# Optimization experiments

Hardware: AMD Instinct MI355X
Metric: run time of the kernel (lower is better)

Reference implementation:

```python
import jax, jax.numpy as jnp
from jax import lax
import numpy as np

N, D, H, ENT = 32768, 16, 128, 50000


def setup_inputs() -> dict:
    key = jax.random.key(0)
    ks = jax.random.split(key, 10)
    s = 0.05  # weight scale to keep tanh/sigmoid in active range
    return {
        "ent_table": jax.random.normal(ks[0], (ENT, H), jnp.float32) * s,
        "op_table": jax.random.normal(ks[1], (5, H), jnp.float32) * s,
        "non_table": jax.random.normal(ks[2], (1, H), jnp.float32) * s,
        "Wm": jax.random.normal(ks[3], (H, 3 * H), jnp.float32) * s,
        "bm": jnp.zeros((H,), jnp.float32),
        "Wg": jax.random.normal(ks[4], (H, 3 * H), jnp.float32) * s,
        "bg": jnp.zeros((H,), jnp.float32),
        "ops_idx": jax.random.randint(ks[5], (N, D), 0, 4, jnp.int32),
        "ents_idx": jax.random.randint(ks[6], (N, D + 1), 0, ENT, jnp.int32),
        "left_idx": jax.random.randint(ks[7], (N,), 0, ENT, jnp.int32),
    }


def reference(ent_table, op_table, non_table, Wm, bm, Wg, bg, ops_idx, ents_idx, left_idx):
    # Merge module (dropout in eval mode = identity):
    #   tanh(Linear([node, t1, t2])) * sigmoid(Linear_g([node, t1, t2]))
    def merge(node, t1, t2):
        x = jnp.concatenate([node, t1, t2], axis=-1)  # [N, 3H]
        return jnp.tanh(x @ Wm.T + bm) * jax.nn.sigmoid(x @ Wg.T + bg)

    op_e = op_table[ops_idx]        # [N, D, H]
    ent_e = ent_table[ents_idx]     # [N, D+1, H]

    # Right-leaning prefix tree: acc starts at deepest entity, merge upward.
    acc0 = ent_e[:, -1]             # [N, H]
    # scan over depth, from innermost (i = D-1) to outermost (i = 0)
    xs = (jnp.flip(op_e, axis=1).transpose(1, 0, 2),          # [D, N, H]
          jnp.flip(ent_e[:, :-1], axis=1).transpose(1, 0, 2))  # [D, N, H]

    def step(acc, inp):
        o, e = inp
        return merge(o, e, acc), None

    acc, _ = lax.scan(step, acc0, xs)

    eq_e = jnp.broadcast_to(op_table[4], acc.shape)  # '=' embedding, [N, H]
    left_e = ent_table[left_idx]                     # [N, H]
    score = merge(eq_e, left_e, acc)                 # [N, H]

    # all_score = cat(per-formula scores, non_embed)  -> [N+1, H]
    return jnp.concatenate([score, non_table], axis=0)
```

## Files before the change

kernel.cpp:

```cpp
#include <hip/hip_runtime.h>
#include <hip/hip_bf16.h>
#include <hip/hip_fp16.h>

#define NROWS 32768
#define HH 128
#define ENTN 50000

typedef _Float16 f16x8 __attribute__((ext_vector_type(8)));
typedef __fp16 fp16x2 __attribute__((ext_vector_type(2)));
typedef float f32x4 __attribute__((ext_vector_type(4)));
typedef float f32x16 __attribute__((ext_vector_type(16)));

#define OFF_PEB 0
#define OFF_WF  25600000
#define OFF_PEF (OFF_WF + 65536)
#define OFF_POPK (OFF_PEF + 65536)

#define KM 2.8853901f
#define KG (-1.4426950f)
#define RSTR 272
#define HALF (32 * RSTR)
#define TILEB (2 * HALF)

#if defined(__has_builtin)
#if __has_builtin(__builtin_amdgcn_exp2f)
#define FEXP2(x) __builtin_amdgcn_exp2f(x)
#endif
#endif
#ifndef FEXP2
__device__ __forceinline__ float __fexp2_asm(float x) {
    float r; asm("v_exp_f32 %0, %1" : "=v"(r) : "v"(x)); return r;
}
#define FEXP2(x) __fexp2_asm(x)
#endif

__device__ __forceinline__ unsigned pk2(float a, float b) {
    fp16x2 h = __builtin_amdgcn_cvt_pkrtz(a, b);
    unsigned u; __builtin_memcpy(&u, &h, 4); return u;
}
__device__ __forceinline__ unsigned pk2rtn(float a, float b) {
    _Float16 lo = (_Float16)a, hi = (_Float16)b;
    unsigned short ul, uh;
    __builtin_memcpy(&ul, &lo, 2); __builtin_memcpy(&uh, &hi, 2);
    return (unsigned)ul | ((unsigned)uh << 16);
}

__global__ void prep_kernel(const float* __restrict__ op_table,
                            const float* __restrict__ non_table,
                            const float* __restrict__ Wm, const float* __restrict__ bm,
                            const float* __restrict__ Wg, const float* __restrict__ bg,
                            char* __restrict__ ws, float* __restrict__ out) {
    int idx = blockIdx.x * blockDim.x + threadIdx.x;
    if (idx < 32768) {
        int e = idx;
        int jj = e & 7, l = (e >> 3) & 63, kt = (e >> 9) & 7, jb = e >> 12;
        int j = jb * 32 + (l & 31);
        int c = j >> 1, p = j & 1;
        int k = kt * 16 + (l >> 5) * 8 + jj;
        const float* Wrow = p ? (Wg + (size_t)c * 384) : (Wm + (size_t)c * 384);
        ((_Float16*)(ws + OFF_WF))[e] = (_Float16)(Wrow[256 + k] * (p ? KG : KM));
    } else if (idx < 65536) {
        int e = idx - 32768;
        int jj = e & 7, l = (e >> 3) & 63, kt = (e >> 9) & 3, jbf = e >> 11;
        int fr = l & 15;
        int j = (jbf >> 1) * 32 + 8 * (fr >> 2) + 4 * (jbf & 1) + (fr & 3);
        int c = j >> 1, p = j & 1;
        int k = kt * 32 + (l >> 4) * 8 + jj;
        const float* Wrow = p ? (Wg + (size_t)c * 384) : (Wm + (size_t)c * 384);
        ((_Float16*)(ws + OFF_PEF))[e] = (_Float16)Wrow[128 + k];
    } else if (idx < 66176) {
        int t2 = idx - 65536;
        int pr = t2 & 1, q = (t2 >> 1) & 3, h = (t2 >> 3) & 1, jb = (t2 >> 4) & 7, o = t2 >> 7;
        int j0 = jb * 32 + 8 * q + 4 * h + 2 * pr;
        int c = j0 >> 1;
        float sm = bm[c], sg = bg[c];
        const float* Wrm = Wm + (size_t)c * 384;
        const float* Wrg = Wg + (size_t)c * 384;
        for (int i = 0; i < 128; ++i) {
            float ov = op_table[o * HH + i];
            sm += ov * Wrm[i];
            sg += ov * Wrg[i];
        }
        ((unsigned*)(ws + OFF_POPK))[t2] = pk2rtn(sm * KM, sg * KG);
    } else if (idx < 66304) {
        int j = idx - 66176;
        out[(size_t)NROWS * HH + j] = non_table[j];
    }
}

__global__ __launch_bounds__(256, 4)
void pe_kernel(const float* __restrict__ ent_table, char* __restrict__ ws) {
    const f16x8* PEF = (const f16x8*)(ws + OFF_PEF);
    char* PEB = ws + OFF_PEB;
    int tid = threadIdx.x, w = tid >> 6, l = tid & 63, lr = l & 15, lg = (l >> 4) & 3;
    int e0 = blockIdx.x * 32;

    f16x8 WB[4][4];
    #pragma unroll
    for (int u = 0; u < 4; ++u)
        #pragma unroll
        for (int kt = 0; kt < 4; ++kt)
            WB[u][kt] = PEF[((4 * w + u) * 4 + kt) * 64 + l];

    f32x4 C[2][4];
    #pragma unroll
    for (int rt = 0; rt < 2; ++rt)
        #pragma unroll
        for (int u = 0; u < 4; ++u) C[rt][u] = (f32x4){0.f, 0.f, 0.f, 0.f};

    #pragma unroll
    for (int kt = 0; kt < 4; ++kt) {
        #pragma unroll
        for (int rt = 0; rt < 2; ++rt) {
            int e = e0 + rt * 16 + lr;
            if (e >= ENTN) e = ENTN - 1;
            const float4* s = (const float4*)(ent_table + (size_t)e * HH + kt * 32 + lg * 8);
            float4 v0 = s[0], v1 = s[1];
            unsigned u4[4] = {pk2(v0.x, v0.y), pk2(v0.z, v0.w),
                              pk2(v1.x, v1.y), pk2(v1.z, v1.w)};
            f16x8 A; __builtin_memcpy(&A, u4, 16);
            #pragma unroll
            for (int u = 0; u < 4; ++u)
                C[rt][u] = __builtin_amdgcn_mfma_f32_16x16x32_f16(WB[u][kt], A, C[rt][u], 0, 0, 0);
        }
    }
    #pragma unroll
    for (int rt = 0; rt < 2; ++rt) {
        int e = e0 + rt * 16 + lr;
        if (e < ENTN) {
            #pragma unroll
            for (int u = 0; u < 4; ++u) {
                int jb2 = 2 * w + (u >> 1);
                uint2 st;
                st.x = pk2(C[rt][u][0] * KM, C[rt][u][1] * KG);
                st.y = pk2(C[rt][u][2] * KM, C[rt][u][3] * KG);
                *(uint2*)(PEB + (size_t)e * 512 + jb2 * 64 + (u & 1) * 32 + lg * 8) = st;
            }
        }
    }
}

__global__ __launch_bounds__(512, 4)
void chain_kernel(const float* __restrict__ ent_table,
                  const int* __restrict__ ops_idx,
                  const int* __restrict__ ents_idx,
                  const int* __restrict__ left_idx,
                  const char* __restrict__ ws, float* __restrict__ out) {
    __shared__ char Abuf[4 * HALF];
    __shared__ unsigned eo[17 * 64];
    __shared__ unsigned popk[640];

    const char* PEBc = ws + OFF_PEB;
    const f16x8* WFp = (const f16x8*)(ws + OFF_WF);
    const unsigned* POPKg = (const unsigned*)(ws + OFF_POPK);

    int tid = threadIdx.x;
    int jb = tid >> 6, l = tid & 63, r = l & 31, h = l >> 5;
    int row0 = blockIdx.x * 64;

    for (int i = tid; i < 17 * 64; i += 512) {
        int t = i >> 6, rr = i & 63;
        unsigned e, o;
        if (t < 16) {
            e = ents_idx[(row0 + rr) * 17 + 15 - t];
            o = ops_idx[(row0 + rr) * 16 + 15 - t];
        } else {
            e = left_idx[row0 + rr];
            o = 4;
        }
        eo[i] = (e << 9) | o;
    }
    for (int i = tid; i < 640; i += 512) popk[i] = POPKg[i];

    f16x8 WH[8];
    #pragma unroll
    for (int kt = 0; kt < 8; ++kt)
        WH[kt] = WFp[(jb * 8 + kt) * 64 + l];

    {
        int rr = tid >> 3, sub = tid & 7;
        int e = ents_idx[(row0 + rr) * 17 + 16];
        const float4* src = (const float4*)(ent_table + (size_t)e * HH + sub * 16);
        float4 a = src[0], b = src[1], c2 = src[2], d2 = src[3];
        uint4 lo, hi;
        lo.x = pk2(a.x, a.y);  lo.y = pk2(a.z, a.w);
        lo.z = pk2(b.x, b.y);  lo.w = pk2(b.z, b.w);
        hi.x = pk2(c2.x, c2.y); hi.y = pk2(c2.z, c2.w);
        hi.z = pk2(d2.x, d2.y); hi.w = pk2(d2.z, d2.w);
        char* dst = Abuf + (rr >> 5) * TILEB + (rr & 31) * RSTR + sub * 32;
        *(uint4*)dst = lo;
        *(uint4*)(dst + 16) = hi;
    }
    __syncthreads();

    int rb = r * RSTR + h * 16;
    int wb = r * RSTR + jb * 32 + h * 4;
    const char* pebBase = PEBc + jb * 64 + h * 32;
    const char* popkB = (const char*)popk + jb * 64 + h * 32;
    const unsigned* eoB = eo + r;

    unsigned vaA = eoB[0], vaB = eoB[32];
    uint4 pa0A = *(const uint4*)(pebBase + (vaA & 0xFFFFFE00u));
    uint4 pa1A = *(const uint4*)(pebBase + (vaA & 0xFFFFFE00u) + 16);
    uint4 pa0B = *(const uint4*)(pebBase + (vaB & 0xFFFFFE00u));
    uint4 pa1B = *(const uint4*)(pebBase + (vaB & 0xFFFFFE00u) + 16);

#define TILE_BODY(VA, PA0, PA1, TOFF, ROWOFF, RD, WR, FINAL)                    \
    {                                                                           \
        const char* pq = popkB + ((VA) & 7u) * 512;                             \
        uint4 po0 = *(const uint4*)(pq);                                        \
        uint4 po1 = *(const uint4*)(pq + 16);                                   \
        unsigned pe_u[8] = {(PA0).x, (PA0).y, (PA0).z, (PA0).w,                 \
                            (PA1).x, (PA1).y, (PA1).z, (PA1).w};                \
        unsigned po_u[8] = {po0.x, po0.y, po0.z, po0.w,                         \
                            po1.x, po1.y, po1.z, po1.w};                        \
        f32x16 C;                                                               \
        _Pragma("unroll")                                                       \
        for (int q = 0; q < 4; ++q)                                             \
            _Pragma("unroll")                                                   \
            for (int pr = 0; pr < 2; ++pr) {                                    \
                int u = q * 2 + pr;                                             \
                __half2 sa = *(const __half2*)&pe_u[u];                         \
                __half2 sb = *(const __half2*)&po_u[u];                         \
                __half2 s = __hadd2(sa, sb);                                    \
                C[4 * q + 2 * pr] = __low2float(s);                             \
                C[4 * q + 2 * pr + 1] = __high2float(s);                        \
            }                                                                   \
        _Pragma("unroll")                                                       \
        for (int kt = 0; kt < 8; ++kt) {                                        \
            f16x8 A = *(const f16x8*)(Abuf + (TOFF) + rb + (RD) + kt * 32);     \
            C = __builtin_amdgcn_mfma_f32_32x32x16_f16(WH[kt], A, C, 0, 0, 0);  \
        }                                                                       \
        _Pragma("unroll")                                                       \
        for (int q = 0; q < 4; ++q) {                                           \
            float ov[2];                                                        \
            _Pragma("unroll")                                                   \
            for (int pr = 0; pr < 2; ++pr) {                                    \
                float m = C[4 * q + 2 * pr];                                    \
                float g = C[4 * q + 2 * pr + 1];                                \
                float em = FEXP2(m), eg = FEXP2(g);                             \
                ov[pr] = (em - 1.f) * __builtin_amdgcn_rcpf((em + 1.f) * (1.f + eg)); \
            }                                                                   \
            if (FINAL) {                                                        \
                *(float2*)(out + (size_t)(row0 + (ROWOFF) + r) * HH             \
                           + jb * 16 + 4 * q + 2 * h) = make_float2(ov[0], ov[1]); \
            } else {                                                            \
                *(unsigned*)(Abuf + (TOFF) + wb + (WR) + q * 8) = pk2(ov[0], ov[1]); \
            }                                                                   \
        }                                                                       \
    }

#define DO_STEP(T, RD, WR, FINAL)                                               \
    {                                                                           \
        uint4 npa0A, npa1A, npa0B, npa1B; unsigned nvaA = 0, nvaB = 0;          \
        if (!(FINAL)) {                                                         \
            nvaA = eoB[((T) + 1) * 64];                                         \
            nvaB = eoB[((T) + 1) * 64 + 32];                                    \
            npa0A = *(const uint4*)(pebBase + (nvaA & 0xFFFFFE00u));            \
            npa1A = *(const uint4*)(pebBase + (nvaA & 0xFFFFFE00u) + 16);       \
            npa0B = *(const uint4*)(pebBase + (nvaB & 0xFFFFFE00u));            \
            npa1B = *(const uint4*)(pebBase + (nvaB & 0xFFFFFE00u) + 16);       \
        }                                                                       \
        TILE_BODY(vaA, pa0A, pa1A, 0, 0, RD, WR, FINAL)                         \
        TILE_BODY(vaB, pa0B, pa1B, TILEB, 32, RD, WR, FINAL)                    \
        __syncthreads();                                                        \
        if (!(FINAL)) {                                                         \
            pa0A = npa0A; pa1A = npa1A; vaA = nvaA;                             \
            pa0B = npa0B; pa1B = npa1B; vaB = nvaB;                             \
        }                                                                       \
    }

    for (int tb = 0; tb < 8; ++tb) {
        int t0 = 2 * tb;
        DO_STEP(t0, 0, HALF, 0)
        DO_STEP(t0 + 1, HALF, 0, 0)
    }
    DO_STEP(16, 0, HALF, 1)
#undef DO_STEP
#undef TILE_BODY
}

extern "C" void kernel_launch(void* const* d_in, const int* in_sizes, int n_in,
                              void* d_out, int out_size, void* d_ws, size_t ws_size,
                              hipStream_t stream) {
    const float* ent_table = (const float*)d_in[0];
    const float* op_table  = (const float*)d_in[1];
    const float* non_table = (const float*)d_in[2];
    const float* Wm        = (const float*)d_in[3];
    const float* bm        = (const float*)d_in[4];
    const float* Wg        = (const float*)d_in[5];
    const float* bg        = (const float*)d_in[6];
    const int* ops_idx     = (const int*)d_in[7];
    const int* ents_idx    = (const int*)d_in[8];
    const int* left_idx    = (const int*)d_in[9];
    float* out = (float*)d_out;
    char* ws = (char*)d_ws;

    prep_kernel<<<259, 256, 0, stream>>>(op_table, non_table, Wm, bm, Wg, bg, ws, out);
    pe_kernel<<<1563, 256, 0, stream>>>(ent_table, ws);
    chain_kernel<<<NROWS / 64, 512, 0, stream>>>(ent_table, ops_idx, ents_idx,
                                                 left_idx, ws, out);
}
```

Measured before the change: 99.79 us.

## Fuse prep and entity-projection kernels into one launch with persistent weight loads

```diff
diff --git a/kernel.cpp b/kernel.cpp
--- a/kernel.cpp
+++ b/kernel.cpp
@@ -5,6 +5,7 @@
 #define NROWS 32768
 #define HH 128
 #define ENTN 50000
+#define PEBLKS 391
 
 typedef _Float16 f16x8 __attribute__((ext_vector_type(8)));
 typedef __fp16 fp16x2 __attribute__((ext_vector_type(2)));
@@ -13,8 +14,7 @@
 
 #define OFF_PEB 0
 #define OFF_WF  25600000
-#define OFF_PEF (OFF_WF + 65536)
-#define OFF_POPK (OFF_PEF + 65536)
+#define OFF_POPK (OFF_WF + 65536)
 
 #define KM 2.8853901f
 #define KG (-1.4426950f)
@@ -45,97 +45,102 @@
     return (unsigned)ul | ((unsigned)uh << 16);
 }
 
-__global__ void prep_kernel(const float* __restrict__ op_table,
-                            const float* __restrict__ non_table,
-                            const float* __restrict__ Wm, const float* __restrict__ bm,
-                            const float* __restrict__ Wg, const float* __restrict__ bg,
-                            char* __restrict__ ws, float* __restrict__ out) {
-    int idx = blockIdx.x * blockDim.x + threadIdx.x;
-    if (idx < 32768) {
-        int e = idx;
-        int jj = e & 7, l = (e >> 3) & 63, kt = (e >> 9) & 7, jb = e >> 12;
-        int j = jb * 32 + (l & 31);
-        int c = j >> 1, p = j & 1;
-        int k = kt * 16 + (l >> 5) * 8 + jj;
-        const float* Wrow = p ? (Wg + (size_t)c * 384) : (Wm + (size_t)c * 384);
-        ((_Float16*)(ws + OFF_WF))[e] = (_Float16)(Wrow[256 + k] * (p ? KG : KM));
-    } else if (idx < 65536) {
-        int e = idx - 32768;
-        int jj = e & 7, l = (e >> 3) & 63, kt = (e >> 9) & 3, jbf = e >> 11;
-        int fr = l & 15;
-        int j = (jbf >> 1) * 32 + 8 * (fr >> 2) + 4 * (jbf & 1) + (fr & 3);
-        int c = j >> 1, p = j & 1;
-        int k = kt * 32 + (l >> 4) * 8 + jj;
-        const float* Wrow = p ? (Wg + (size_t)c * 384) : (Wm + (size_t)c * 384);
-        ((_Float16*)(ws + OFF_PEF))[e] = (_Float16)Wrow[128 + k];
-    } else if (idx < 66176) {
-        int t2 = idx - 65536;
-        int pr = t2 & 1, q = (t2 >> 1) & 3, h = (t2 >> 3) & 1, jb = (t2 >> 4) & 7, o = t2 >> 7;
-        int j0 = jb * 32 + 8 * q + 4 * h + 2 * pr;
-        int c = j0 >> 1;
-        float sm = bm[c], sg = bg[c];
-        const float* Wrm = Wm + (size_t)c * 384;
-        const float* Wrg = Wg + (size_t)c * 384;
-        for (int i = 0; i < 128; ++i) {
-            float ov = op_table[o * HH + i];
-            sm += ov * Wrm[i];
-            sg += ov * Wrg[i];
+__global__ __launch_bounds__(256, 4)
+void pe_prep_kernel(const float* __restrict__ ent_table,
+                    const float* __restrict__ op_table,
+                    const float* __restrict__ non_table,
+                    const float* __restrict__ Wm, const float* __restrict__ bm,
+                    const float* __restrict__ Wg, const float* __restrict__ bg,
+                    char* __restrict__ ws, float* __restrict__ out) {
+    int blk = blockIdx.x;
+    int tid = threadIdx.x;
+    if (blk < PEBLKS) {
+        char* PEB = ws + OFF_PEB;
+        int w = tid >> 6, l = tid & 63, lr = l & 15, lg = (l >> 4) & 3;
+
+        f16x8 WB[4][4];
+        #pragma unroll
+        for (int u = 0; u < 4; ++u) {
+            int jbf = 4 * w + u;
+            int j = (jbf >> 1) * 32 + 8 * (lr >> 2) + 4 * (jbf & 1) + (lr & 3);
+            int c = j >> 1, p = j & 1;
+            const float* Wrow = (p ? Wg : Wm) + (size_t)c * 384 + 128;
+            #pragma unroll
+            for (int kt = 0; kt < 4; ++kt) {
+                const float4* s = (const float4*)(Wrow + kt * 32 + lg * 8);
+                float4 a0 = s[0], a1 = s[1];
+                _Float16 h8[8] = {(_Float16)a0.x, (_Float16)a0.y, (_Float16)a0.z, (_Float16)a0.w,
+                                  (_Float16)a1.x, (_Float16)a1.y, (_Float16)a1.z, (_Float16)a1.w};
+                WB[u][kt] = *(f16x8*)h8;
+            }
         }
-        ((unsigned*)(ws + OFF_POPK))[t2] = pk2rtn(sm * KM, sg * KG);
-    } else if (idx < 66304) {
-        int j = idx - 66176;
-        out[(size_t)NROWS * HH + j] = non_table[j];
-    }
-}
-
-__global__ __launch_bounds__(256, 4)
-void pe_kernel(const float* __restrict__ ent_table, char* __restrict__ ws) {
-    const f16x8* PEF = (const f16x8*)(ws + OFF_PEF);
-    char* PEB = ws + OFF_PEB;
-    int tid = threadIdx.x, w = tid >> 6, l = tid & 63, lr = l & 15, lg = (l >> 4) & 3;
-    int e0 = blockIdx.x * 32;
-
-    f16x8 WB[4][4];
-    #pragma unroll
-    for (int u = 0; u < 4; ++u)
-        #pragma unroll
-        for (int kt = 0; kt < 4; ++kt)
-            WB[u][kt] = PEF[((4 * w + u) * 4 + kt) * 64 + l];
-
-    f32x4 C[2][4];
-    #pragma unroll
-    for (int rt = 0; rt < 2; ++rt)
-        #pragma unroll
-        for (int u = 0; u < 4; ++u) C[rt][u] = (f32x4){0.f, 0.f, 0.f, 0.f};
-
-    #pragma unroll
-    for (int kt = 0; kt < 4; ++kt) {
-        #pragma unroll
-        for (int rt = 0; rt < 2; ++rt) {
-            int e = e0 + rt * 16 + lr;
-            if (e >= ENTN) e = ENTN - 1;
-            const float4* s = (const float4*)(ent_table + (size_t)e * HH + kt * 32 + lg * 8);
-            float4 v0 = s[0], v1 = s[1];
-            unsigned u4[4] = {pk2(v0.x, v0.y), pk2(v0.z, v0.w),
-                              pk2(v1.x, v1.y), pk2(v1.z, v1.w)};
-            f16x8 A; __builtin_memcpy(&A, u4, 16);
+
+        for (int it = 0; it < 4; ++it) {
+            int e0 = blk * 128 + it * 32;
+            f32x4 C[2][4];
             #pragma unroll
-            for (int u = 0; u < 4; ++u)
-                C[rt][u] = __builtin_amdgcn_mfma_f32_16x16x32_f16(WB[u][kt], A, C[rt][u], 0, 0, 0);
+            for (int rt = 0; rt < 2; ++rt)
+                #pragma unroll
+                for (int u = 0; u < 4; ++u) C[rt][u] = (f32x4){0.f, 0.f, 0.f, 0.f};
+
+            #pragma unroll
+            for (int kt = 0; kt < 4; ++kt) {
+                #pragma unroll
+                for (int rt = 0; rt < 2; ++rt) {
+                    int e = e0 + rt * 16 + lr;
+                    if (e >= ENTN) e = ENTN - 1;
+                    const float4* s = (const float4*)(ent_table + (size_t)e * HH + kt * 32 + lg * 8);
+                    float4 v0 = s[0], v1 = s[1];
+                    unsigned u4[4] = {pk2(v0.x, v0.y), pk2(v0.z, v0.w),
+                                      pk2(v1.x, v1.y), pk2(v1.z, v1.w)};
+                    f16x8 A; __builtin_memcpy(&A, u4, 16);
+                    #pragma unroll
+                    for (int u = 0; u < 4; ++u)
+                        C[rt][u] = __builtin_amdgcn_mfma_f32_16x16x32_f16(WB[u][kt], A, C[rt][u], 0, 0, 0);
+                }
+            }
+            #pragma unroll
+            for (int rt = 0; rt < 2; ++rt) {
+                int e = e0 + rt * 16 + lr;
+                if (e < ENTN) {
+                    #pragma unroll
+                    for (int u = 0; u < 4; ++u) {
+                        int jb2 = 2 * w + (u >> 1);
+                        uint2 st;
+                        st.x = pk2(C[rt][u][0] * KM, C[rt][u][1] * KG);
+                        st.y = pk2(C[rt][u][2] * KM, C[rt][u][3] * KG);
+                        *(uint2*)(PEB + (size_t)e * 512 + jb2 * 64 + (u & 1) * 32 + lg * 8) = st;
+                    }
+                }
+            }
         }
-    }
-    #pragma unroll
-    for (int rt = 0; rt < 2; ++rt) {
-        int e = e0 + rt * 16 + lr;
-        if (e < ENTN) {
-            #pragma unroll
-            for (int u = 0; u < 4; ++u) {
-                int jb2 = 2 * w + (u >> 1);
-                uint2 st;
-                st.x = pk2(C[rt][u][0] * KM, C[rt][u][1] * KG);
-                st.y = pk2(C[rt][u][2] * KM, C[rt][u][3] * KG);
-                *(uint2*)(PEB + (size_t)e * 512 + jb2 * 64 + (u & 1) * 32 + lg * 8) = st;
+    } else {
+        int idx = (blk - PEBLKS) * 256 + tid;
+        if (idx < 32768) {
+            int e = idx;
+            int jj = e & 7, l = (e >> 3) & 63, kt = (e >> 9) & 7, jb = e >> 12;
+            int j = jb * 32 + (l & 31);
+            int c = j >> 1, p = j & 1;
+            int k = kt * 16 + (l >> 5) * 8 + jj;
+            const float* Wrow = p ? (Wg + (size_t)c * 384) : (Wm + (size_t)c * 384);
+            ((_Float16*)(ws + OFF_WF))[e] = (_Float16)(Wrow[256 + k] * (p ? KG : KM));
+        } else if (idx < 33408) {
+            int t2 = idx - 32768;
+            int pr = t2 & 1, q = (t2 >> 1) & 3, h = (t2 >> 3) & 1, jb = (t2 >> 4) & 7, o = t2 >> 7;
+            int j0 = jb * 32 + 8 * q + 4 * h + 2 * pr;
+            int c = j0 >> 1;
+            float sm = bm[c], sg = bg[c];
+            const float* Wrm = Wm + (size_t)c * 384;
+            const float* Wrg = Wg + (size_t)c * 384;
+            for (int i = 0; i < 128; ++i) {
+                float ov = op_table[o * HH + i];
+                sm += ov * Wrm[i];
+                sg += ov * Wrg[i];
             }
+            ((unsigned*)(ws + OFF_POPK))[t2] = pk2rtn(sm * KM, sg * KG);
+        } else if (idx < 33536) {
+            int j = idx - 33408;
+            out[(size_t)NROWS * HH + j] = non_table[j];
         }
     }
 }
@@ -296,8 +301,8 @@
     float* out = (float*)d_out;
     char* ws = (char*)d_ws;
 
-    prep_kernel<<<259, 256, 0, stream>>>(op_table, non_table, Wm, bm, Wg, bg, ws, out);
-    pe_kernel<<<1563, 256, 0, stream>>>(ent_table, ws);
+    pe_prep_kernel<<<PEBLKS + 131, 256, 0, stream>>>(ent_table, op_table, non_table,
+                                                     Wm, bm, Wg, bg, ws, out);
     chain_kernel<<<NROWS / 64, 512, 0, stream>>>(ent_table, ops_idx, ents_idx,
                                                  left_idx, ws, out);
 }
```

Result: slower. 104.1 us (+4.3%).
